# Kernel optimization log

Hardware: AMD Instinct MI355X
Metric: run time of the kernel (lower is better)

Reference implementation:

```python
import jax, jax.numpy as jnp
import numpy as np

B, T = 1024, 8192
NUM_WORDS = 2048  # ph2word.max() + 1, forced by construction in setup_inputs
OFFSET = 1.0
LAMBDA_P, LAMBDA_W, LAMBDA_S = 0.6, 0.3, 0.1
RULES_SCALE = 0.3
INIT_TOKENS = np.array([94, 122, 100, 92, 43, 27], dtype=np.int32)
INIT_DURS = np.array([2.0, 3.0, 2.0, 2.0, 5.0, 5.0], dtype=np.float32)
RATIO_TOKENS = np.array([44, 28, 29, 27, 121, 43], dtype=np.int32)


def setup_inputs() -> dict:
    key = jax.random.key(0)
    k1, k2, k3, k4 = jax.random.split(key, 4)
    dur_pred = jax.random.uniform(k1, (B, T), dtype=jnp.float32) * 10.0
    dur_gt = jax.random.uniform(k2, (B, T), dtype=jnp.float32) * 10.0
    ph2word = jnp.sort(jax.random.randint(k3, (B, T), 0, NUM_WORDS, dtype=jnp.int32), axis=1)
    ph2word = ph2word.at[:, -1].set(NUM_WORDS - 1)  # guarantee max == NUM_WORDS-1 (static shape)
    txt_tokens = jax.random.randint(k4, (B, T), 0, 150, dtype=jnp.int32)
    return {"dur_pred": dur_pred, "dur_gt": dur_gt, "ph2word": ph2word, "txt_tokens": txt_tokens}


def _linear2log(x):
    return jnp.log(x + OFFSET)


def _mse(a, b):
    d = a - b
    return jnp.mean(d * d)


def _dur_rules(dur_pred, txt_tokens):
    # Vectorized form of the sequential double loop. At step i the carry value
    # dur_rules[:, i] is unconditionally reset to dur_pred[:, i], so the ratio
    # rule's forward write to i+1 never survives; final value is
    #   dur_pred[i] - self_adjust(i) + neighbor_gaps_from(i+1).
    tok = txt_tokens[..., None]  # [B,T,1]
    in_init = jnp.any(tok == jnp.asarray(INIT_TOKENS), axis=-1)
    expected = jnp.sum(jnp.where(tok == jnp.asarray(INIT_TOKENS), jnp.asarray(INIT_DURS), 0.0), axis=-1)
    gap1 = dur_pred - expected
    fire1 = in_init & (gap1 > 0)
    gap1 = jnp.where(fire1, gap1, 0.0)

    in_ratio = jnp.any(tok == jnp.asarray(RATIO_TOKENS), axis=-1)
    dp_next = jnp.concatenate([dur_pred[:, 1:], jnp.zeros_like(dur_pred[:, :1])], axis=1)
    valid_next = jnp.arange(dur_pred.shape[1]) < dur_pred.shape[1] - 1
    fire2 = in_ratio & valid_next[None, :] & (3.0 * dur_pred > dp_next)
    gap2 = jnp.where(fire2, dur_pred - dp_next / 3.0, 0.0)

    # ratio rule overwrites (not adds to) the self position when it fires
    self_adj = jnp.where(fire2, gap2, jnp.where(fire1, gap1, 0.0))
    dur_rules = dur_pred - self_adj
    # gaps from iteration i+1 are added to position i (only for i+1 >= 1, always true)
    dur_rules = dur_rules.at[:, :-1].add((gap1 + gap2)[:, 1:])
    return dur_rules


def reference(dur_pred, dur_gt, ph2word, txt_tokens):
    dur_gt = dur_gt.astype(dur_pred.dtype)

    dur_rules = _dur_rules(dur_pred, txt_tokens)
    rules_loss = RULES_SCALE * _mse(_linear2log(dur_pred), _linear2log(dur_rules))

    pdur_loss = LAMBDA_P * _mse(_linear2log(dur_pred), _linear2log(dur_gt))

    dp_c = jnp.maximum(dur_pred, 0.0)
    seg = lambda d, s: jax.ops.segment_sum(d, s, num_segments=NUM_WORDS)
    wdur_pred = jax.vmap(seg)(dp_c, ph2word)[:, 1:]
    wdur_gt = jax.vmap(seg)(dur_gt, ph2word)[:, 1:]
    wdur_loss = LAMBDA_W * _mse(_linear2log(wdur_pred), _linear2log(wdur_gt))

    sdur_pred = jnp.sum(dp_c, axis=1)
    sdur_gt = jnp.sum(dur_gt, axis=1)
    sdur_loss = LAMBDA_S * _mse(_linear2log(sdur_pred), _linear2log(sdur_gt))

    return pdur_loss + wdur_loss + sdur_loss + rules_loss
```

## Files before the change

### kernel.cpp

```cpp
#include <hip/hip_runtime.h>

constexpr int Bn  = 1024;
constexpr int Tn  = 8192;
constexpr int Wn  = 2048;
constexpr int TPB = 512;
constexpr int BPR = 4;
constexpr int SEG = Tn / BPR;

__device__ __forceinline__ void rule_eval(float dp, float dpn, int tok, bool valid_next,
                                          float& g1, float& g2, float& sa) {
  float expected;
  bool in_init = true;
  switch (tok) {
    case 94:  expected = 2.f; break;
    case 122: expected = 3.f; break;
    case 100: expected = 2.f; break;
    case 92:  expected = 2.f; break;
    case 43:  expected = 5.f; break;
    case 27:  expected = 5.f; break;
    default:  expected = 0.f; in_init = false; break;
  }
  float t1 = dp - expected;
  bool fire1 = in_init && (t1 > 0.f);
  g1 = fire1 ? t1 : 0.f;
  bool in_ratio = (tok == 44) | (tok == 28) | (tok == 29) |
                  (tok == 27) | (tok == 121) | (tok == 43);
  bool fire2 = in_ratio && valid_next && (3.f * dp > dpn);
  g2 = fire2 ? (dp - dpn * (1.f / 3.f)) : 0.f;
  sa = fire2 ? g2 : (fire1 ? g1 : 0.f);
}

__device__ __forceinline__ float wave_reduce(float v) {
  #pragma unroll
  for (int o = 32; o > 0; o >>= 1) v += __shfl_down(v, o, 64);
  return v;
}

__global__ __launch_bounds__(TPB, 8) void loss_kernel(
    const float* __restrict__ dur_pred, const float* __restrict__ dur_gt,
    const int* __restrict__ ph2word, const int* __restrict__ txt,
    float4* __restrict__ partials)
{
  __shared__ float wp[Wn];
  __shared__ float wg[Wn];
  __shared__ float sacc[5];
  __shared__ int   smeta[2];

  const int row = blockIdx.x >> 2;
  const int sub = blockIdx.x & 3;
  const int s = sub * SEG;
  const size_t roff = (size_t)row * Tn;
  const float* __restrict__ dpr = dur_pred + roff;
  const float* __restrict__ dgr = dur_gt + roff;
  const int*   __restrict__ pwr = ph2word + roff;
  const int*   __restrict__ tkr = txt + roff;

  const int tid  = threadIdx.x;
  const int lane = tid & 63;
  const bool is63 = (lane == 63);
  const int base = s + tid * 4;

  float4 dp4 = *reinterpret_cast<const float4*>(dpr + base);
  float4 dg4 = *reinterpret_cast<const float4*>(dgr + base);
  int4   pw4 = *reinterpret_cast<const int4*>(pwr + base);
  int4   tk4 = *reinterpret_cast<const int4*>(tkr + base);

  float nb_dp = 0.f, nb_dp1 = 0.f; int nb_tk = -1;
  if (is63) {
    const int p = base + 4;
    if (p < Tn) { nb_dp = dpr[p]; nb_dp1 = dpr[p + 1]; nb_tk = tkr[p]; }
  }

  if (tid == 0)       smeta[0] = pw4.x;
  if (tid == TPB - 1) smeta[1] = pw4.w;

  {
    const float4 z = {0.f, 0.f, 0.f, 0.f};
    *reinterpret_cast<float4*>(&wp[tid * 4]) = z;
    *reinterpret_cast<float4*>(&wg[tid * 4]) = z;
  }
  if (tid < 5) sacc[tid] = 0.f;
  __syncthreads();

  float g1v[4], g2v[4], sav[4];
  rule_eval(dp4.x, dp4.y, tk4.x, true, g1v[0], g2v[0], sav[0]);
  rule_eval(dp4.y, dp4.z, tk4.y, true, g1v[1], g2v[1], sav[1]);
  rule_eval(dp4.z, dp4.w, tk4.z, true, g1v[2], g2v[2], sav[2]);
  float gg0 = g1v[0] + g2v[0];

  float dpn3 = __shfl_down(dp4.x, 1, 64);
  float ggn  = __shfl_down(gg0,  1, 64);
  {
    float ng1, ng2, nsa_;
    rule_eval(nb_dp, nb_dp1, nb_tk, base + 4 < Tn - 1, ng1, ng2, nsa_);
    dpn3 = is63 ? nb_dp : dpn3;
    ggn  = is63 ? (ng1 + ng2) : ggn;
  }
  rule_eval(dp4.w, dpn3, tk4.w, base + 3 < Tn - 1, g1v[3], g2v[3], sav[3]);

  float dpx[4] = {dp4.x, dp4.y, dp4.z, dp4.w};
  float dgl[4] = {dg4.x, dg4.y, dg4.z, dg4.w};
  float addv[4] = {g1v[1] + g2v[1], g1v[2] + g2v[2], g1v[3] + g2v[3],
                   (base + 3 < Tn - 1) ? ggn : 0.f};

  float pdur_s = 0.f, rules_s = 0.f, sp = 0.f, sg = 0.f;
  #pragma unroll
  for (int j = 0; j < 4; ++j) {
    float dp = dpx[j];
    float dr = dp - sav[j] + addv[j];
    float lp = __logf(dp + 1.f);
    float dlr = lp - __logf(dr + 1.f);
    rules_s += dlr * dlr;
    float dlg = lp - __logf(dgl[j] + 1.f);
    pdur_s += dlg * dlg;
    sp += fmaxf(dp, 0.f);
    sg += dgl[j];
  }

  {
    int pwl[4] = {pw4.x, pw4.y, pw4.z, pw4.w};
    int curw = pwl[0];
    float ap = 0.f, ag = 0.f;
    #pragma unroll
    for (int j = 0; j < 4; ++j) {
      if (pwl[j] != curw) {
        atomicAdd(&wp[curw], ap);
        atomicAdd(&wg[curw], ag);
        curw = pwl[j]; ap = 0.f; ag = 0.f;
      }
      ap += fmaxf(dpx[j], 0.f);
      ag += dgl[j];
    }
    atomicAdd(&wp[curw], ap);
    atomicAdd(&wg[curw], ag);
  }

  __syncthreads();

  const int wf = smeta[0];
  const int wl = smeta[1];

  float wd_s = 0.f;
  for (int w = wf + 1 + tid; w < wl; w += TPB) {
    float d = __logf(wp[w] + 1.f) - __logf(wg[w] + 1.f);
    wd_s += d * d;
  }

  pdur_s  = wave_reduce(pdur_s);
  rules_s = wave_reduce(rules_s);
  sp      = wave_reduce(sp);
  sg      = wave_reduce(sg);
  wd_s    = wave_reduce(wd_s);
  if (lane == 0) {
    atomicAdd(&sacc[0], pdur_s);
    atomicAdd(&sacc[1], rules_s);
    atomicAdd(&sacc[2], sp);
    atomicAdd(&sacc[3], sg);
    atomicAdd(&sacc[4], wd_s);
  }
  __syncthreads();

  if (tid == 0) {
    float4 a, b, c;
    a.x = sacc[0]; a.y = sacc[1]; a.z = sacc[4]; a.w = sacc[2];
    b.x = sacc[3];
    if (wf != wl) { b.y = wp[wf]; b.z = wg[wf]; b.w = __int_as_float(wf); }
    else          { b.y = 0.f;    b.z = 0.f;    b.w = __int_as_float(-1); }
    c.x = wp[wl]; c.y = wg[wl]; c.z = __int_as_float(wl); c.w = 0.f;
    const size_t idx = (size_t)blockIdx.x * 3;
    partials[idx]     = a;
    partials[idx + 1] = b;
    partials[idx + 2] = c;
  }
}

__global__ __launch_bounds__(1024) void finalize_kernel(
    const float4* __restrict__ partials, float* __restrict__ out)
{
  __shared__ double wsum[16];
  const int r = threadIdx.x;
  double pd = 0.0, rl = 0.0, wd = 0.0;
  float sp = 0.f, sg = 0.f;
  int curid = -1; float cp = 0.f, cg = 0.f;

  #pragma unroll
  for (int j = 0; j < BPR; ++j) {
    const size_t idx = ((size_t)r * BPR + j) * 3;
    float4 a = partials[idx];
    float4 b = partials[idx + 1];
    float4 c = partials[idx + 2];
    pd += (double)a.x; rl += (double)a.y; wd += (double)a.z;
    sp += a.w; sg += b.x;
    const int wfi = __float_as_int(b.w);
    const int wla = __float_as_int(c.z);
    if (wfi >= 0) {
      if (wfi != curid) {
        if (curid > 0) { float d = __logf(cp + 1.f) - __logf(cg + 1.f); wd += (double)(d * d); }
        curid = wfi; cp = 0.f; cg = 0.f;
      }
      cp += b.y; cg += b.z;
    }
    if (wla >= 0) {
      if (wla != curid) {
        if (curid > 0) { float d = __logf(cp + 1.f) - __logf(cg + 1.f); wd += (double)(d * d); }
        curid = wla; cp = 0.f; cg = 0.f;
      }
      cp += c.x; cg += c.y;
    }
  }
  if (curid > 0) { float d = __logf(cp + 1.f) - __logf(cg + 1.f); wd += (double)(d * d); }

  float ds = __logf(sp + 1.f) - __logf(sg + 1.f);
  double contrib = 0.6 * pd / ((double)Bn * (double)Tn)
                 + 0.3 * rl / ((double)Bn * (double)Tn)
                 + 0.3 * wd / ((double)Bn * (double)(Wn - 1))
                 + 0.1 * (double)(ds * ds) / (double)Bn;

  #pragma unroll
  for (int o = 32; o > 0; o >>= 1) contrib += __shfl_down(contrib, o, 64);
  if ((threadIdx.x & 63) == 0) wsum[threadIdx.x >> 6] = contrib;
  __syncthreads();
  if (threadIdx.x == 0) {
    double t = 0.0;
    #pragma unroll
    for (int i = 0; i < 16; ++i) t += wsum[i];
    out[0] = (float)t;
  }
}

extern "C" void kernel_launch(void* const* d_in, const int* in_sizes, int n_in,
                              void* d_out, int out_size, void* d_ws, size_t ws_size,
                              hipStream_t stream) {
  const float* dur_pred = (const float*)d_in[0];
  const float* dur_gt   = (const float*)d_in[1];
  const int*   ph2word  = (const int*)d_in[2];
  const int*   txt      = (const int*)d_in[3];

  float4* partials = (float4*)d_ws;

  loss_kernel<<<Bn * BPR, TPB, 0, stream>>>(dur_pred, dur_gt, ph2word, txt, partials);
  finalize_kernel<<<1, 1024, 0, stream>>>(partials, (float*)d_out);
}
```

Before: 181.1 us.

## Replace LDS word histogram with wave-level segmented scan over sorted word ids

Drops the per-block 2048-entry shared-memory word accumulators, which had to be zeroed, filled with LDS atomics and then scanned. Because ph2word is sorted, per-word sums are instead built with wave shuffles: a prefix scan, a ballot to find segment starts, and a small cross-wave carry through shared memory. Each thread's completed words feed the log-MSE directly, and only block-boundary words are passed on to the finalize kernel. Blocks shrink to 256 threads with 8 blocks per row, and the loss terms are pre-weighted into one partial. This removes LDS traffic and allows higher occupancy, at the cost of more intricate segment-boundary logic and a larger finalize workload.

```diff
diff --git a/kernel.cpp b/kernel.cpp
--- a/kernel.cpp
+++ b/kernel.cpp
@@ -3,9 +3,11 @@
 constexpr int Bn  = 1024;
 constexpr int Tn  = 8192;
 constexpr int Wn  = 2048;
-constexpr int TPB = 512;
-constexpr int BPR = 4;
-constexpr int SEG = Tn / BPR;
+constexpr int TPB = 256;
+constexpr int NW  = TPB / 64;
+constexpr int SEG = TPB * 4;
+constexpr int BPR = Tn / SEG;
+constexpr float WDC = 0.3f * (float)Tn / (float)(Wn - 1);
 
 __device__ __forceinline__ void rule_eval(float dp, float dpn, int tok, bool valid_next,
                                           float& g1, float& g2, float& sa) {
@@ -36,18 +38,23 @@
   return v;
 }
 
-__global__ __launch_bounds__(TPB, 8) void loss_kernel(
+__global__ __launch_bounds__(TPB, 6) void loss_kernel(
     const float* __restrict__ dur_pred, const float* __restrict__ dur_gt,
     const int* __restrict__ ph2word, const int* __restrict__ txt,
     float4* __restrict__ partials)
 {
-  __shared__ float wp[Wn];
-  __shared__ float wg[Wn];
-  __shared__ float sacc[5];
+  __shared__ int   hk[NW];
+  __shared__ float ndp0[NW], ndp1[NW];
+  __shared__ int   ntk[NW];
+  __shared__ int   twk[NW];
+  __shared__ float twp[NW], twg[NW];
+  __shared__ int   wu_[NW];
+  __shared__ float bnd[4];
   __shared__ int   smeta[2];
-
-  const int row = blockIdx.x >> 2;
-  const int sub = blockIdx.x & 3;
+  __shared__ float red[NW][3];
+
+  const int row = blockIdx.x / BPR;
+  const int sub = blockIdx.x % BPR;
   const int s = sub * SEG;
   const size_t roff = (size_t)row * Tn;
   const float* __restrict__ dpr = dur_pred + roff;
@@ -57,6 +64,7 @@
 
   const int tid  = threadIdx.x;
   const int lane = tid & 63;
+  const int wid  = tid >> 6;
   const bool is63 = (lane == 63);
   const int base = s + tid * 4;
 
@@ -66,44 +74,101 @@
   int4   tk4 = *reinterpret_cast<const int4*>(tkr + base);
 
   float nb_dp = 0.f, nb_dp1 = 0.f; int nb_tk = -1;
-  if (is63) {
+  if (tid == TPB - 1) {
     const int p = base + 4;
     if (p < Tn) { nb_dp = dpr[p]; nb_dp1 = dpr[p + 1]; nb_tk = tkr[p]; }
   }
 
-  if (tid == 0)       smeta[0] = pw4.x;
-  if (tid == TPB - 1) smeta[1] = pw4.w;
-
-  {
-    const float4 z = {0.f, 0.f, 0.f, 0.f};
-    *reinterpret_cast<float4*>(&wp[tid * 4]) = z;
-    *reinterpret_cast<float4*>(&wg[tid * 4]) = z;
-  }
-  if (tid < 5) sacc[tid] = 0.f;
-  __syncthreads();
+  const int k0 = pw4.x, k1 = pw4.y, k2 = pw4.z, k3 = pw4.w;
+  const float p0 = fmaxf(dp4.x, 0.f), p1 = fmaxf(dp4.y, 0.f),
+              p2 = fmaxf(dp4.z, 0.f), p3 = fmaxf(dp4.w, 0.f);
+  const float g0 = dg4.x, g1_ = dg4.y, g2_ = dg4.z, g3_ = dg4.w;
+  const float Sp = p0 + p1 + p2 + p3;
+  const float Sg = g0 + g1_ + g2_ + g3_;
+
+  float t3p = p3, t3g = g3_;
+  if (k2 == k3) { t3p += p2; t3g += g2_;
+    if (k1 == k3) { t3p += p1; t3g += g1_;
+      if (k0 == k3) { t3p += p0; t3g += g0; } } }
+
+  float Pp = Sp, Pg = Sg;
+  #pragma unroll
+  for (int o = 1; o < 64; o <<= 1) {
+    float tp = __shfl_up(Pp, o, 64);
+    float tg = __shfl_up(Pg, o, 64);
+    if (lane >= o) { Pp += tp; Pg += tg; }
+  }
+
+  const int nk0 = __shfl_down(k0, 1, 64);
+  const bool uni = (k0 == k3);
+  const bool cn  = uni && (k3 == nk0);
+  const unsigned long long cmask = __ballot(cn);
+  const unsigned long long below = (1ull << lane) - 1ull;
+  const unsigned long long y = (~cmask) & below;
+  const int L = y ? (64 - __clzll(y)) : 0;
+  const int Lm1 = (L > 0) ? (L - 1) : 0;
+  const float Ppm1 = __shfl_up(Pp, 1, 64);
+  const float Pgm1 = __shfl_up(Pg, 1, 64);
+  const float PpL = __shfl(Pp, Lm1, 64);
+  const float PgL = __shfl(Pg, Lm1, 64);
+  const int   k3L = __shfl(k3, Lm1, 64);
+  const float tpL = __shfl(t3p, Lm1, 64);
+  const float tgL = __shfl(t3g, Lm1, 64);
+  float Cp = 0.f, Cg = 0.f;
+  if (L < lane) {
+    Cp = Ppm1 - (L > 0 ? PpL : 0.f);
+    Cg = Pgm1 - (L > 0 ? PgL : 0.f);
+  }
+  if (L > 0 && k3L == k0) {
+    Cp += tpL; Cg += tgL;
+  }
+  const bool open = (y == 0);
 
   float g1v[4], g2v[4], sav[4];
   rule_eval(dp4.x, dp4.y, tk4.x, true, g1v[0], g2v[0], sav[0]);
   rule_eval(dp4.y, dp4.z, tk4.y, true, g1v[1], g2v[1], sav[1]);
   rule_eval(dp4.z, dp4.w, tk4.z, true, g1v[2], g2v[2], sav[2]);
   float gg0 = g1v[0] + g2v[0];
-
   float dpn3 = __shfl_down(dp4.x, 1, 64);
   float ggn  = __shfl_down(gg0,  1, 64);
+
+  if (lane == 0) { hk[wid] = k0; ndp0[wid] = dp4.x; ndp1[wid] = dp4.y; ntk[wid] = tk4.x; }
+  if (is63) {
+    twk[wid] = k3;
+    twp[wid] = uni ? (Cp + Sp) : t3p;
+    twg[wid] = uni ? (Cg + Sg) : t3g;
+    wu_[wid] = (uni && open) ? 1 : 0;
+  }
+  if (tid == 0) { smeta[0] = k0; bnd[0] = 0.f; bnd[1] = 0.f; bnd[2] = 0.f; bnd[3] = 0.f; }
+  if (tid == TPB - 1) smeta[1] = k3;
+  __syncthreads();
+
   {
-    float ng1, ng2, nsa_;
-    rule_eval(nb_dp, nb_dp1, nb_tk, base + 4 < Tn - 1, ng1, ng2, nsa_);
-    dpn3 = is63 ? nb_dp : dpn3;
-    ggn  = is63 ? (ng1 + ng2) : ggn;
+    const int myh = hk[wid];
+    float Wp = 0.f, Wg = 0.f;
+    for (int u = wid - 1; u >= 0; --u) {
+      if (twk[u] != myh) break;
+      Wp += twp[u]; Wg += twg[u];
+      if (!wu_[u]) break;
+    }
+    if (open) { Cp += Wp; Cg += Wg; }
+  }
+
+  if (is63) {
+    float a0, a1; int t0;
+    if (tid == TPB - 1) { a0 = nb_dp; a1 = nb_dp1; t0 = nb_tk; }
+    else                { a0 = ndp0[wid + 1]; a1 = ndp1[wid + 1]; t0 = ntk[wid + 1]; }
+    float ng1, ng2, ns_;
+    rule_eval(a0, a1, t0, base + 4 < Tn - 1, ng1, ng2, ns_);
+    dpn3 = a0; ggn = ng1 + ng2;
   }
   rule_eval(dp4.w, dpn3, tk4.w, base + 3 < Tn - 1, g1v[3], g2v[3], sav[3]);
 
   float dpx[4] = {dp4.x, dp4.y, dp4.z, dp4.w};
-  float dgl[4] = {dg4.x, dg4.y, dg4.z, dg4.w};
+  float dgl[4] = {g0, g1_, g2_, g3_};
   float addv[4] = {g1v[1] + g2v[1], g1v[2] + g2v[2], g1v[3] + g2v[3],
                    (base + 3 < Tn - 1) ? ggn : 0.f};
-
-  float pdur_s = 0.f, rules_s = 0.f, sp = 0.f, sg = 0.f;
+  float pdur_s = 0.f, rules_s = 0.f;
   #pragma unroll
   for (int j = 0; j < 4; ++j) {
     float dp = dpx[j];
@@ -113,60 +178,48 @@
     rules_s += dlr * dlr;
     float dlg = lp - __logf(dgl[j] + 1.f);
     pdur_s += dlg * dlg;
-    sp += fmaxf(dp, 0.f);
-    sg += dgl[j];
-  }
-
+  }
+
+  const int wf = smeta[0], wl = smeta[1];
+  const int nk_true = is63 ? ((tid == TPB - 1) ? -1 : hk[wid + 1]) : nk0;
+  float wd_s = 0.f;
   {
-    int pwl[4] = {pw4.x, pw4.y, pw4.z, pw4.w};
-    int curw = pwl[0];
-    float ap = 0.f, ag = 0.f;
+    const int   kk[4] = {k0, k1, k2, k3};
+    const float pp[4] = {p0, p1, p2, p3};
+    const float gg[4] = {g0, g1_, g2_, g3_};
+    int cur = k0; float ap = Cp, ag = Cg;
     #pragma unroll
     for (int j = 0; j < 4; ++j) {
-      if (pwl[j] != curw) {
-        atomicAdd(&wp[curw], ap);
-        atomicAdd(&wg[curw], ag);
-        curw = pwl[j]; ap = 0.f; ag = 0.f;
+      if (kk[j] != cur) {
+        if (cur == wl)      { bnd[2] = ap; bnd[3] = ag; }
+        else if (cur == wf) { bnd[0] = ap; bnd[1] = ag; }
+        else { float d = __logf(ap + 1.f) - __logf(ag + 1.f); wd_s += d * d; }
+        cur = kk[j]; ap = 0.f; ag = 0.f;
       }
-      ap += fmaxf(dpx[j], 0.f);
-      ag += dgl[j];
-    }
-    atomicAdd(&wp[curw], ap);
-    atomicAdd(&wg[curw], ag);
-  }
-
+      ap += pp[j]; ag += gg[j];
+    }
+    if (nk_true != cur) {
+      if (cur == wl)      { bnd[2] = ap; bnd[3] = ag; }
+      else if (cur == wf) { bnd[0] = ap; bnd[1] = ag; }
+      else { float d = __logf(ap + 1.f) - __logf(ag + 1.f); wd_s += d * d; }
+    }
+  }
+
+  float x = 0.6f * pdur_s + 0.3f * rules_s + WDC * wd_s;
+  x = wave_reduce(x);
+  if (lane == 0) red[wid][0] = x;
+  if (is63) { red[wid][1] = Pp; red[wid][2] = Pg; }
   __syncthreads();
 
-  const int wf = smeta[0];
-  const int wl = smeta[1];
-
-  float wd_s = 0.f;
-  for (int w = wf + 1 + tid; w < wl; w += TPB) {
-    float d = __logf(wp[w] + 1.f) - __logf(wg[w] + 1.f);
-    wd_s += d * d;
-  }
-
-  pdur_s  = wave_reduce(pdur_s);
-  rules_s = wave_reduce(rules_s);
-  sp      = wave_reduce(sp);
-  sg      = wave_reduce(sg);
-  wd_s    = wave_reduce(wd_s);
-  if (lane == 0) {
-    atomicAdd(&sacc[0], pdur_s);
-    atomicAdd(&sacc[1], rules_s);
-    atomicAdd(&sacc[2], sp);
-    atomicAdd(&sacc[3], sg);
-    atomicAdd(&sacc[4], wd_s);
-  }
-  __syncthreads();
-
   if (tid == 0) {
+    float xs = 0.f, sp = 0.f, sg = 0.f;
+    #pragma unroll
+    for (int w = 0; w < NW; ++w) { xs += red[w][0]; sp += red[w][1]; sg += red[w][2]; }
     float4 a, b, c;
-    a.x = sacc[0]; a.y = sacc[1]; a.z = sacc[4]; a.w = sacc[2];
-    b.x = sacc[3];
-    if (wf != wl) { b.y = wp[wf]; b.z = wg[wf]; b.w = __int_as_float(wf); }
-    else          { b.y = 0.f;    b.z = 0.f;    b.w = __int_as_float(-1); }
-    c.x = wp[wl]; c.y = wg[wl]; c.z = __int_as_float(wl); c.w = 0.f;
+    a.x = xs; a.y = sp; a.z = sg; a.w = 0.f;
+    const bool single = (wf == wl);
+    b.x = bnd[0]; b.y = bnd[1]; b.z = __int_as_float(single ? -1 : wf); b.w = 0.f;
+    c.x = bnd[2]; c.y = bnd[3]; c.z = __int_as_float(wl); c.w = 0.f;
     const size_t idx = (size_t)blockIdx.x * 3;
     partials[idx]     = a;
     partials[idx + 1] = b;
@@ -179,7 +232,7 @@
 {
   __shared__ double wsum[16];
   const int r = threadIdx.x;
-  double pd = 0.0, rl = 0.0, wd = 0.0;
+  double xs = 0.0, wdb = 0.0;
   float sp = 0.f, sg = 0.f;
   int curid = -1; float cp = 0.f, cg = 0.f;
 
@@ -189,31 +242,29 @@
     float4 a = partials[idx];
     float4 b = partials[idx + 1];
     float4 c = partials[idx + 2];
-    pd += (double)a.x; rl += (double)a.y; wd += (double)a.z;
-    sp += a.w; sg += b.x;
-    const int wfi = __float_as_int(b.w);
+    xs += (double)a.x; sp += a.y; sg += a.z;
+    const int wfi = __float_as_int(b.z);
     const int wla = __float_as_int(c.z);
     if (wfi >= 0) {
       if (wfi != curid) {
-        if (curid > 0) { float d = __logf(cp + 1.f) - __logf(cg + 1.f); wd += (double)(d * d); }
+        if (curid > 0) { float d = __logf(cp + 1.f) - __logf(cg + 1.f); wdb += (double)(d * d); }
         curid = wfi; cp = 0.f; cg = 0.f;
       }
-      cp += b.y; cg += b.z;
+      cp += b.x; cg += b.y;
     }
     if (wla >= 0) {
       if (wla != curid) {
-        if (curid > 0) { float d = __logf(cp + 1.f) - __logf(cg + 1.f); wd += (double)(d * d); }
+        if (curid > 0) { float d = __logf(cp + 1.f) - __logf(cg + 1.f); wdb += (double)(d * d); }
         curid = wla; cp = 0.f; cg = 0.f;
       }
       cp += c.x; cg += c.y;
     }
   }
-  if (curid > 0) { float d = __logf(cp + 1.f) - __logf(cg + 1.f); wd += (double)(d * d); }
+  if (curid > 0) { float d = __logf(cp + 1.f) - __logf(cg + 1.f); wdb += (double)(d * d); }
 
   float ds = __logf(sp + 1.f) - __logf(sg + 1.f);
-  double contrib = 0.6 * pd / ((double)Bn * (double)Tn)
-                 + 0.3 * rl / ((double)Bn * (double)Tn)
-                 + 0.3 * wd / ((double)Bn * (double)(Wn - 1))
+  double contrib = xs / ((double)Bn * (double)Tn)
+                 + 0.3 * wdb / ((double)Bn * (double)(Wn - 1))
                  + 0.1 * (double)(ds * ds) / (double)Bn;
 
   #pragma unroll
```

After: 167.7 us. -7.4%, faster.
